# Kernel tuning notes

Measured on AMD Instinct MI355X. Metric: run time of the kernel, lower is better.

The kernel has to match this reference:

```python
import jax, jax.numpy as jnp
import numpy as np

# Dimensions
O, D, F_LSOA = 128, 128, 64      # origins, destinations, LSOA feature dim
T, FE, H = 128, 16, 64           # max seq len, edge_feature_dim, gru_hidden
NH, NO, PH = 128, 64, 128        # node_hidden, node_out, pair_hidden
P = O * D                        # number of O-D pairs


def _mlp3(x, W1, b1, W2, b2, W3, b3):
    # Linear->ReLU->Linear->ReLU->Linear (dropout is identity in eval mode)
    h = jax.nn.relu(x @ W1 + b1)
    h = jax.nn.relu(h @ W2 + b2)
    return h @ W3 + b3


def setup_inputs() -> dict:
    key = jax.random.key(0)
    ks = jax.random.split(key, 32)

    def rn(k, shape, s):
        return jax.random.normal(k, shape, dtype=jnp.float32) * s

    inp = {
        "O_feats": rn(ks[0], (O, F_LSOA), 1.0),
        "D_feats": rn(ks[1], (D, F_LSOA), 1.0),
        "seqs": rn(ks[2], (P, T, FE), 1.0),
        "lengths": jax.random.randint(ks[3], (P,), 1, T + 1, dtype=jnp.int32),
        # enc_O
        "WO1": rn(ks[4], (F_LSOA, NH), 0.05), "bO1": jnp.zeros((NH,), jnp.float32),
        "WO2": rn(ks[5], (NH, NH), 0.05),     "bO2": jnp.zeros((NH,), jnp.float32),
        "WO3": rn(ks[6], (NH, NO), 0.05),     "bO3": jnp.zeros((NO,), jnp.float32),
        # enc_D
        "WD1": rn(ks[7], (F_LSOA, NH), 0.05), "bD1": jnp.zeros((NH,), jnp.float32),
        "WD2": rn(ks[8], (NH, NH), 0.05),     "bD2": jnp.zeros((NH,), jnp.float32),
        "WD3": rn(ks[9], (NH, NO), 0.05),     "bD3": jnp.zeros((NO,), jnp.float32),
        # pair_head: 2*node_out -> pair_hidden -> 1
        "Wp1": rn(ks[10], (2 * NO, PH), 0.05), "bp1": jnp.zeros((PH,), jnp.float32),
        "Wp2": rn(ks[11], (PH, 1), 0.05),      "bp2": jnp.zeros((1,), jnp.float32),
        # GRU (gate order r, z, n as in PyTorch)
        "W_ih": rn(ks[12], (FE, 3 * H), 0.1),  "b_ih": jnp.zeros((3 * H,), jnp.float32),
        "W_hh": rn(ks[13], (H, 3 * H), 0.1),   "b_hh": jnp.zeros((3 * H,), jnp.float32),
        # seq_head
        "Ws": rn(ks[14], (H, 1), 0.1),         "bs": jnp.zeros((1,), jnp.float32),
    }
    return inp


def reference(O_feats, D_feats, seqs, lengths,
              WO1, bO1, WO2, bO2, WO3, bO3,
              WD1, bD1, WD2, bD2, WD3, bD3,
              Wp1, bp1, Wp2, bp2,
              W_ih, W_hh, b_ih, b_hh,
              Ws, bs):
    # Node encoders
    eo = _mlp3(O_feats, WO1, bO1, WO2, bO2, WO3, bO3)   # [O, NO]
    ed = _mlp3(D_feats, WD1, bD1, WD2, bD2, WD3, bD3)   # [D, NO]

    # Pairwise score: concat(eo, ed) -> MLP -> softplus
    pair_in = jnp.concatenate([
        jnp.broadcast_to(eo[:, None, :], (O, D, NO)),
        jnp.broadcast_to(ed[None, :, :], (O, D, NO)),
    ], axis=-1)                                          # [O, D, 2*NO]
    hp = jax.nn.relu(pair_in @ Wp1 + bp1)                # [O, D, PH]
    z_pair = (hp @ Wp2 + bp2)[..., 0]                    # [O, D]
    s_pair = jax.nn.softplus(z_pair)

    # Length-masked GRU over all O*D padded sequences (equiv. to pack_padded)
    xT = jnp.swapaxes(seqs, 0, 1)                        # [T, P, FE]
    h0 = jnp.zeros((P, H), jnp.float32)

    def step(h, inp):
        xt, t = inp
        gx = xt @ W_ih + b_ih                            # [P, 3H]
        gh = h @ W_hh + b_hh                             # [P, 3H]
        xr, xz, xn = jnp.split(gx, 3, axis=-1)
        hr, hz, hn = jnp.split(gh, 3, axis=-1)
        r = jax.nn.sigmoid(xr + hr)
        zg = jax.nn.sigmoid(xz + hz)
        n = jnp.tanh(xn + r * hn)
        h_new = (1.0 - zg) * n + zg * h
        h = jnp.where((t < lengths)[:, None], h_new, h)  # freeze past seq end
        return h, None

    h_last, _ = jax.lax.scan(step, h0, (xT, jnp.arange(T)))  # [P, H]

    p_seq = jax.nn.sigmoid(h_last @ Ws + bs)[:, 0].reshape(O, D)
    return jnp.sum(s_pair * p_seq)
```

## Files before the change

### kernel.cpp

```cpp
#include <hip/hip_runtime.h>
#include <hip/hip_bf16.h>

#define O_N 128
#define D_N 128
#define F_LS 64
#define T_MAX 128
#define FE_N 16
#define H_GRU 64
#define NH 128
#define NO 64
#define PH 128
#define NG 1024

typedef _Float16 f16;
typedef f16 f16x8 __attribute__((ext_vector_type(8)));
typedef f16 f16x4 __attribute__((ext_vector_type(4)));
typedef float f32x4 __attribute__((ext_vector_type(4)));

__device__ __forceinline__ float fast_sigmoid(float x) {
    return __builtin_amdgcn_rcpf(1.f + __expf(-x));
}
__device__ __forceinline__ float fast_tanh(float x) {
    return 1.f - 2.f * __builtin_amdgcn_rcpf(1.f + __expf(2.f * x));
}

__global__ __launch_bounds__(128) void k_enc(
    const float* __restrict__ O_feats, const float* __restrict__ D_feats,
    const float* __restrict__ WO1, const float* __restrict__ bO1,
    const float* __restrict__ WO2, const float* __restrict__ bO2,
    const float* __restrict__ WO3, const float* __restrict__ bO3,
    const float* __restrict__ WD1, const float* __restrict__ bD1,
    const float* __restrict__ WD2, const float* __restrict__ bD2,
    const float* __restrict__ WD3, const float* __restrict__ bD3,
    const float* __restrict__ Wp1,
    float* __restrict__ PA, float* __restrict__ PB, float* __restrict__ d_out)
{
    __shared__ float h1[NH];
    __shared__ float h2[NH];
    __shared__ float ev[NO];
    const int b = blockIdx.x;
    const int enc = b >> 7;
    const int row = b & 127;
    const int t = threadIdx.x;
    if (b == 0 && t == 0) d_out[0] = 0.f;

    const float* x  = (enc ? D_feats : O_feats) + row * F_LS;
    const float* W1 = enc ? WD1 : WO1;  const float* b1 = enc ? bD1 : bO1;
    const float* W2 = enc ? WD2 : WO2;  const float* b2 = enc ? bD2 : bO2;
    const float* W3 = enc ? WD3 : WO3;  const float* b3 = enc ? bD3 : bO3;

    float a = b1[t];
    #pragma unroll 8
    for (int k = 0; k < F_LS; ++k) a += x[k] * W1[k * NH + t];
    h1[t] = fmaxf(a, 0.f);
    __syncthreads();

    a = b2[t];
    #pragma unroll 8
    for (int k = 0; k < NH; ++k) a += h1[k] * W2[k * NH + t];
    h2[t] = fmaxf(a, 0.f);
    __syncthreads();

    if (t < NO) {
        a = b3[t];
        #pragma unroll 8
        for (int k = 0; k < NH; ++k) a += h2[k] * W3[k * NO + t];
        ev[t] = a;
    }
    __syncthreads();

    const float* Wp = Wp1 + (enc ? NO * PH : 0);
    a = 0.f;
    #pragma unroll 8
    for (int k = 0; k < NO; ++k) a += ev[k] * Wp[k * PH + t];
    (enc ? PB : PA)[row * PH + t] = a;
}

__global__ __launch_bounds__(128) void k_pair(
    const float* __restrict__ PA, const float* __restrict__ PB,
    const float* __restrict__ bp1, const float* __restrict__ Wp2,
    const float* __restrict__ bp2, float* __restrict__ s_pair)
{
    const int i = blockIdx.x;
    const int j = threadIdx.x;
    __shared__ float pa[PH];
    __shared__ float b1s[PH];
    __shared__ float w2s[PH];
    pa[j]  = PA[i * PH + j];
    b1s[j] = bp1[j];
    w2s[j] = Wp2[j];
    __syncthreads();
    const float* pb = PB + j * PH;
    float acc = 0.f;
    #pragma unroll 8
    for (int c = 0; c < PH; ++c)
        acc += w2s[c] * fmaxf(pa[c] + pb[c] + b1s[c], 0.f);
    float z = acc + bp2[0];
    float sp = fmaxf(z, 0.f) + log1pf(__expf(-fabsf(z)));
    s_pair[i * 128 + j] = sp;
}

__global__ __launch_bounds__(1024) void k_sort(
    const int* __restrict__ lengths, int* __restrict__ perm)
{
    __shared__ int cnt[130];
    __shared__ int suf[130];
    const int t = threadIdx.x;
    if (t < 130) cnt[t] = 0;
    __syncthreads();
    for (int i = t; i < 16384; i += 1024) atomicAdd(&cnt[lengths[i]], 1);
    __syncthreads();
    if (t < 130) suf[t] = cnt[t];
    __syncthreads();
    for (int d = 1; d < 130; d <<= 1) {
        int v = 0;
        if (t < 130) { v = suf[t]; if (t + d < 130) v += suf[t + d]; }
        __syncthreads();
        if (t < 130) suf[t] = v;
        __syncthreads();
    }
    if (t < 129) cnt[t] = (t + 1 < 130) ? suf[t + 1] : 0;
    __syncthreads();
    for (int i = t; i < 16384; i += 1024) {
        int pos = atomicAdd(&cnt[lengths[i]], 1);
        perm[pos] = i;
    }
}

__global__ __launch_bounds__(256, 2) void k_gru(
    const float* __restrict__ seqs, const int* __restrict__ lengths,
    const int* __restrict__ perm,
    const float* __restrict__ W_ih, const float* __restrict__ b_ih,
    const float* __restrict__ W_hh, const float* __restrict__ b_hh,
    const float* __restrict__ Ws, const float* __restrict__ bs,
    const float* __restrict__ s_pair, float* __restrict__ d_out)
{
    __shared__ __align__(16) f16 hbuf[2 * 16 * 72];
    __shared__ float red[64];
    const int tid = threadIdx.x;
    const int w  = tid >> 6;
    const int l  = tid & 63;
    const int q  = l >> 4;
    const int n  = l & 15;
    const int c  = w * 16 + n;
    const f32x4 zero4 = {0.f, 0.f, 0.f, 0.f};
    const f16x8 zero8 = {(f16)0, (f16)0, (f16)0, (f16)0, (f16)0, (f16)0, (f16)0, (f16)0};

    f16x8 wh[3][2], wi[3];
    #pragma unroll
    for (int g = 0; g < 3; ++g) {
        const int gb = g * 64;
        #pragma unroll
        for (int ks = 0; ks < 2; ++ks)
            #pragma unroll
            for (int j = 0; j < 8; ++j)
                wh[g][ks][j] = (f16)W_hh[(ks * 32 + q * 8 + j) * 192 + gb + c];
        #pragma unroll
        for (int j = 0; j < 8; ++j) {
            int k = q * 8 + j;
            wi[g][j] = (k < FE_N) ? (f16)W_ih[k * 192 + gb + c] : (f16)0.f;
        }
    }
    const float brz_r = b_ih[c] + b_hh[c];
    const float brz_z = b_ih[64 + c] + b_hh[64 + c];
    const float bxn   = b_ih[128 + c];
    const float bhn   = b_hh[128 + c];
    const float wsc   = Ws[c];
    const float bsv   = bs[0];

    for (int gi = 0; gi < 2; ++gi) {
        const int g  = gi ? (NG - 1 - (int)blockIdx.x) : (int)blockIdx.x;
        const int pb = g * 16;

        int pr[4], len[4];
        #pragma unroll
        for (int r = 0; r < 4; ++r) {
            pr[r]  = perm[pb + q * 4 + r];
            len[r] = lengths[pr[r]];
        }
        int ml = max(max(len[0], len[1]), max(len[2], len[3]));
        ml = max(ml, __shfl_xor(ml, 16));
        ml = max(ml, __shfl_xor(ml, 32));
        const int maxlen = __builtin_amdgcn_readfirstlane(ml);

        if (tid < 144) *(f16x8*)&hbuf[tid * 8] = zero8;

        const int pp = perm[pb + n];
        const float4* xp = (const float4*)(seqs + (size_t)pp * (T_MAX * FE_N)) + q * 2;
        float4 xa = {0.f, 0.f, 0.f, 0.f}, xb = xa;
        if (q < 2) { xa = xp[0]; xb = xp[1]; }

        float hold[4] = {0.f, 0.f, 0.f, 0.f};
        __syncthreads();

        for (int t = 0; t < maxlen; ++t) {
            f16x8 ax = zero8;
            if (q < 2) {
                ax[0] = (f16)xa.x; ax[1] = (f16)xa.y; ax[2] = (f16)xa.z; ax[3] = (f16)xa.w;
                ax[4] = (f16)xb.x; ax[5] = (f16)xb.y; ax[6] = (f16)xb.z; ax[7] = (f16)xb.w;
                int tn = (t + 1 < maxlen) ? (t + 1) : t;
                xa = xp[tn * 4];
                xb = xp[tn * 4 + 1];
            }
            const f16* hb  = hbuf + (t & 1) * 1152;
            f16*       hbn = hbuf + ((t + 1) & 1) * 1152;

            f16x8 ah0 = *(const f16x8*)&hb[n * 72 + q * 8];
            f16x8 ah1 = *(const f16x8*)&hb[n * 72 + 32 + q * 8];

            f32x4 axn = __builtin_amdgcn_mfma_f32_16x16x32_f16(ax, wi[2], zero4, 0, 0, 0);
            f32x4 ar  = __builtin_amdgcn_mfma_f32_16x16x32_f16(ax, wi[0], zero4, 0, 0, 0);
            ar  = __builtin_amdgcn_mfma_f32_16x16x32_f16(ah0, wh[0][0], ar, 0, 0, 0);
            ar  = __builtin_amdgcn_mfma_f32_16x16x32_f16(ah1, wh[0][1], ar, 0, 0, 0);
            f32x4 az  = __builtin_amdgcn_mfma_f32_16x16x32_f16(ax, wi[1], zero4, 0, 0, 0);
            az  = __builtin_amdgcn_mfma_f32_16x16x32_f16(ah0, wh[1][0], az, 0, 0, 0);
            az  = __builtin_amdgcn_mfma_f32_16x16x32_f16(ah1, wh[1][1], az, 0, 0, 0);
            f32x4 ahn = __builtin_amdgcn_mfma_f32_16x16x32_f16(ah0, wh[2][0], zero4, 0, 0, 0);
            ahn = __builtin_amdgcn_mfma_f32_16x16x32_f16(ah1, wh[2][1], ahn, 0, 0, 0);

            #pragma unroll
            for (int r = 0; r < 4; ++r) {
                float rg   = fast_sigmoid(ar[r] + brz_r);
                float zg   = fast_sigmoid(az[r] + brz_z);
                float nn   = fast_tanh(fmaf(rg, ahn[r] + bhn, axn[r] + bxn));
                float hnew = fmaf(zg, hold[r] - nn, nn);
                hnew = (t < len[r]) ? hnew : hold[r];
                hold[r] = hnew;
                hbn[(q * 4 + r) * 72 + c] = (f16)hnew;
            }
            __syncthreads();
        }

        float part[4];
        #pragma unroll
        for (int r = 0; r < 4; ++r) part[r] = hold[r] * wsc;
        #pragma unroll
        for (int off = 1; off < 16; off <<= 1)
            #pragma unroll
            for (int r = 0; r < 4; ++r)
                part[r] += __shfl_xor(part[r], off);
        if (n == 0) {
            #pragma unroll
            for (int r = 0; r < 4; ++r) red[w * 16 + q * 4 + r] = part[r];
        }
        __syncthreads();
        if (tid < 16) {
            float s = red[tid] + red[16 + tid] + red[32 + tid] + red[48 + tid];
            float pv = fast_sigmoid(s + bsv);
            float contrib = s_pair[perm[pb + tid]] * pv;
            #pragma unroll
            for (int off = 1; off < 16; off <<= 1)
                contrib += __shfl_xor(contrib, off);
            if (tid == 0) atomicAdd(d_out, contrib);
        }
    }
}

extern "C" void kernel_launch(void* const* d_in, const int* in_sizes, int n_in,
                              void* d_out, int out_size, void* d_ws, size_t ws_size,
                              hipStream_t stream)
{
    const float* O_feats = (const float*)d_in[0];
    const float* D_feats = (const float*)d_in[1];
    const float* seqs    = (const float*)d_in[2];
    const int*   lengths = (const int*)d_in[3];
    const float* WO1 = (const float*)d_in[4];  const float* bO1 = (const float*)d_in[5];
    const float* WO2 = (const float*)d_in[6];  const float* bO2 = (const float*)d_in[7];
    const float* WO3 = (const float*)d_in[8];  const float* bO3 = (const float*)d_in[9];
    const float* WD1 = (const float*)d_in[10]; const float* bD1 = (const float*)d_in[11];
    const float* WD2 = (const float*)d_in[12]; const float* bD2 = (const float*)d_in[13];
    const float* WD3 = (const float*)d_in[14]; const float* bD3 = (const float*)d_in[15];
    const float* Wp1 = (const float*)d_in[16]; const float* bp1 = (const float*)d_in[17];
    const float* Wp2 = (const float*)d_in[18]; const float* bp2 = (const float*)d_in[19];
    const float* W_ih = (const float*)d_in[20]; const float* b_ih = (const float*)d_in[21];
    const float* W_hh = (const float*)d_in[22]; const float* b_hh = (const float*)d_in[23];
    const float* Ws   = (const float*)d_in[24]; const float* bs   = (const float*)d_in[25];

    float* out    = (float*)d_out;
    float* PA     = (float*)d_ws;
    float* PB     = PA + 128 * 128;
    float* s_pair = PB + 128 * 128;
    int*   perm   = (int*)(s_pair + 16384);

    k_enc<<<256, 128, 0, stream>>>(O_feats, D_feats,
                                   WO1, bO1, WO2, bO2, WO3, bO3,
                                   WD1, bD1, WD2, bD2, WD3, bD3,
                                   Wp1, PA, PB, out);
    k_pair<<<128, 128, 0, stream>>>(PA, PB, bp1, Wp2, bp2, s_pair);
    k_sort<<<1, 1024, 0, stream>>>(lengths, perm);
    k_gru<<<512, 256, 0, stream>>>(seqs, lengths, perm, W_ih, b_ih, W_hh, b_hh,
                                   Ws, bs, s_pair, out);
}
```

Measured before the change: 391.6 us.

## Launch one GRU block per group with higher occupancy and pre-scaled gate weights

The GRU kernel now launches 1024 blocks, one per 16-sequence group, instead of 512 blocks that each process a paired short and long group, and raises the occupancy hint to 4 blocks per SM. Gate weights and biases are pre-scaled by -log2(e) and 2*log2(e), so the activations use raw exp2 and rcp, and the biases are folded into the MFMA accumulator initial values. This removes per-element adds and multiplies on the serial recurrence path and exposes more concurrent waves to hide latency. In exchange, it drops the load balancing from pairing groups and risks register spills under the tighter occupancy bound.

New measurement: 372.0 us. 5.0% less time.

```diff
diff --git a/kernel.cpp b/kernel.cpp
--- a/kernel.cpp
+++ b/kernel.cpp
@@ -14,14 +14,10 @@
 
 typedef _Float16 f16;
 typedef f16 f16x8 __attribute__((ext_vector_type(8)));
-typedef f16 f16x4 __attribute__((ext_vector_type(4)));
 typedef float f32x4 __attribute__((ext_vector_type(4)));
 
 __device__ __forceinline__ float fast_sigmoid(float x) {
     return __builtin_amdgcn_rcpf(1.f + __expf(-x));
-}
-__device__ __forceinline__ float fast_tanh(float x) {
-    return 1.f - 2.f * __builtin_amdgcn_rcpf(1.f + __expf(2.f * x));
 }
 
 __global__ __launch_bounds__(128) void k_enc(
@@ -127,7 +123,7 @@
     }
 }
 
-__global__ __launch_bounds__(256, 2) void k_gru(
+__global__ __launch_bounds__(256, 4) void k_gru(
     const float* __restrict__ seqs, const int* __restrict__ lengths,
     const int* __restrict__ perm,
     const float* __restrict__ W_ih, const float* __restrict__ b_ih,
@@ -135,7 +131,7 @@
     const float* __restrict__ Ws, const float* __restrict__ bs,
     const float* __restrict__ s_pair, float* __restrict__ d_out)
 {
-    __shared__ __align__(16) f16 hbuf[2 * 16 * 72];
+    __shared__ __align__(16) f16 hbuf[2 * 1152];
     __shared__ float red[64];
     const int tid = threadIdx.x;
     const int w  = tid >> 6;
@@ -143,116 +139,120 @@
     const int q  = l >> 4;
     const int n  = l & 15;
     const int c  = w * 16 + n;
-    const f32x4 zero4 = {0.f, 0.f, 0.f, 0.f};
-    const f16x8 zero8 = {(f16)0, (f16)0, (f16)0, (f16)0, (f16)0, (f16)0, (f16)0, (f16)0};
+    const int pb = blockIdx.x * 16;
+    const float S_RZ = -1.4426950408889634f;
+    const float S_N  =  2.8853900817779268f;
 
     f16x8 wh[3][2], wi[3];
     #pragma unroll
     for (int g = 0; g < 3; ++g) {
         const int gb = g * 64;
+        const float s = (g < 2) ? S_RZ : S_N;
         #pragma unroll
         for (int ks = 0; ks < 2; ++ks)
             #pragma unroll
             for (int j = 0; j < 8; ++j)
-                wh[g][ks][j] = (f16)W_hh[(ks * 32 + q * 8 + j) * 192 + gb + c];
+                wh[g][ks][j] = (f16)(W_hh[(ks * 32 + q * 8 + j) * 192 + gb + c] * s);
         #pragma unroll
         for (int j = 0; j < 8; ++j) {
             int k = q * 8 + j;
-            wi[g][j] = (k < FE_N) ? (f16)W_ih[k * 192 + gb + c] : (f16)0.f;
+            wi[g][j] = (k < FE_N) ? (f16)(W_ih[k * 192 + gb + c] * s) : (f16)0.f;
         }
     }
-    const float brz_r = b_ih[c] + b_hh[c];
-    const float brz_z = b_ih[64 + c] + b_hh[64 + c];
-    const float bxn   = b_ih[128 + c];
-    const float bhn   = b_hh[128 + c];
-    const float wsc   = Ws[c];
-    const float bsv   = bs[0];
-
-    for (int gi = 0; gi < 2; ++gi) {
-        const int g  = gi ? (NG - 1 - (int)blockIdx.x) : (int)blockIdx.x;
-        const int pb = g * 16;
-
-        int pr[4], len[4];
+    const float brz_r = S_RZ * (b_ih[c] + b_hh[c]);
+    const float brz_z = S_RZ * (b_ih[64 + c] + b_hh[64 + c]);
+    const float bhn_s = S_N * b_hh[128 + c];
+    const float bxn_s = S_N * b_ih[128 + c];
+    const f32x4 c_r  = {brz_r, brz_r, brz_r, brz_r};
+    const f32x4 c_z  = {brz_z, brz_z, brz_z, brz_z};
+    const f32x4 c_hn = {bhn_s, bhn_s, bhn_s, bhn_s};
+    const f32x4 c_xn = {bxn_s, bxn_s, bxn_s, bxn_s};
+    const float wsc  = Ws[c];
+    const float bsv  = bs[0];
+
+    int len[4];
+    #pragma unroll
+    for (int r = 0; r < 4; ++r) len[r] = lengths[perm[pb + q * 4 + r]];
+    int ml = max(max(len[0], len[1]), max(len[2], len[3]));
+    ml = max(ml, __shfl_xor(ml, 16));
+    ml = max(ml, __shfl_xor(ml, 32));
+    const int maxlen = __builtin_amdgcn_readfirstlane(ml);
+
+    {
+        f16x8 z8 = {(f16)0, (f16)0, (f16)0, (f16)0, (f16)0, (f16)0, (f16)0, (f16)0};
+        if (tid < 144) *(f16x8*)&hbuf[tid * 8] = z8;
+    }
+
+    const int pp = perm[pb + n];
+    const float4* xp = (const float4*)(seqs + (size_t)pp * (T_MAX * FE_N)) + q * 2;
+    float4 xa = {0.f, 0.f, 0.f, 0.f}, xb = xa;
+    if (q < 2) { xa = xp[0]; xb = xp[1]; }
+
+    float hold[4] = {0.f, 0.f, 0.f, 0.f};
+    const f16x8 zero8 = {(f16)0, (f16)0, (f16)0, (f16)0, (f16)0, (f16)0, (f16)0, (f16)0};
+    __syncthreads();
+
+    for (int t = 0; t < maxlen; ++t) {
+        f16x8 ax = zero8;
+        if (q < 2) {
+            ax[0] = (f16)xa.x; ax[1] = (f16)xa.y; ax[2] = (f16)xa.z; ax[3] = (f16)xa.w;
+            ax[4] = (f16)xb.x; ax[5] = (f16)xb.y; ax[6] = (f16)xb.z; ax[7] = (f16)xb.w;
+            int tn = (t + 1 < maxlen) ? (t + 1) : t;
+            xa = xp[tn * 4];
+            xb = xp[tn * 4 + 1];
+        }
+        const f16* hb  = hbuf + (t & 1) * 1152;
+        f16*       hbn = hbuf + ((t + 1) & 1) * 1152;
+
+        f16x8 ah0 = *(const f16x8*)&hb[n * 72 + q * 8];
+        f16x8 ah1 = *(const f16x8*)&hb[n * 72 + 32 + q * 8];
+
+        f32x4 ar = __builtin_amdgcn_mfma_f32_16x16x32_f16(ah0, wh[0][0], c_r, 0, 0, 0);
+        ar = __builtin_amdgcn_mfma_f32_16x16x32_f16(ah1, wh[0][1], ar, 0, 0, 0);
+        ar = __builtin_amdgcn_mfma_f32_16x16x32_f16(ax,  wi[0],    ar, 0, 0, 0);
+        f32x4 az = __builtin_amdgcn_mfma_f32_16x16x32_f16(ah0, wh[1][0], c_z, 0, 0, 0);
+        az = __builtin_amdgcn_mfma_f32_16x16x32_f16(ah1, wh[1][1], az, 0, 0, 0);
+        az = __builtin_amdgcn_mfma_f32_16x16x32_f16(ax,  wi[1],    az, 0, 0, 0);
+        f32x4 hn = __builtin_amdgcn_mfma_f32_16x16x32_f16(ah0, wh[2][0], c_hn, 0, 0, 0);
+        hn = __builtin_amdgcn_mfma_f32_16x16x32_f16(ah1, wh[2][1], hn, 0, 0, 0);
+        f32x4 xn = __builtin_amdgcn_mfma_f32_16x16x32_f16(ax, wi[2], c_xn, 0, 0, 0);
+
         #pragma unroll
         for (int r = 0; r < 4; ++r) {
-            pr[r]  = perm[pb + q * 4 + r];
-            len[r] = lengths[pr[r]];
-        }
-        int ml = max(max(len[0], len[1]), max(len[2], len[3]));
-        ml = max(ml, __shfl_xor(ml, 16));
-        ml = max(ml, __shfl_xor(ml, 32));
-        const int maxlen = __builtin_amdgcn_readfirstlane(ml);
-
-        if (tid < 144) *(f16x8*)&hbuf[tid * 8] = zero8;
-
-        const int pp = perm[pb + n];
-        const float4* xp = (const float4*)(seqs + (size_t)pp * (T_MAX * FE_N)) + q * 2;
-        float4 xa = {0.f, 0.f, 0.f, 0.f}, xb = xa;
-        if (q < 2) { xa = xp[0]; xb = xp[1]; }
-
-        float hold[4] = {0.f, 0.f, 0.f, 0.f};
-        __syncthreads();
-
-        for (int t = 0; t < maxlen; ++t) {
-            f16x8 ax = zero8;
-            if (q < 2) {
-                ax[0] = (f16)xa.x; ax[1] = (f16)xa.y; ax[2] = (f16)xa.z; ax[3] = (f16)xa.w;
-                ax[4] = (f16)xb.x; ax[5] = (f16)xb.y; ax[6] = (f16)xb.z; ax[7] = (f16)xb.w;
-                int tn = (t + 1 < maxlen) ? (t + 1) : t;
-                xa = xp[tn * 4];
-                xb = xp[tn * 4 + 1];
-            }
-            const f16* hb  = hbuf + (t & 1) * 1152;
-            f16*       hbn = hbuf + ((t + 1) & 1) * 1152;
-
-            f16x8 ah0 = *(const f16x8*)&hb[n * 72 + q * 8];
-            f16x8 ah1 = *(const f16x8*)&hb[n * 72 + 32 + q * 8];
-
-            f32x4 axn = __builtin_amdgcn_mfma_f32_16x16x32_f16(ax, wi[2], zero4, 0, 0, 0);
-            f32x4 ar  = __builtin_amdgcn_mfma_f32_16x16x32_f16(ax, wi[0], zero4, 0, 0, 0);
-            ar  = __builtin_amdgcn_mfma_f32_16x16x32_f16(ah0, wh[0][0], ar, 0, 0, 0);
-            ar  = __builtin_amdgcn_mfma_f32_16x16x32_f16(ah1, wh[0][1], ar, 0, 0, 0);
-            f32x4 az  = __builtin_amdgcn_mfma_f32_16x16x32_f16(ax, wi[1], zero4, 0, 0, 0);
-            az  = __builtin_amdgcn_mfma_f32_16x16x32_f16(ah0, wh[1][0], az, 0, 0, 0);
-            az  = __builtin_amdgcn_mfma_f32_16x16x32_f16(ah1, wh[1][1], az, 0, 0, 0);
-            f32x4 ahn = __builtin_amdgcn_mfma_f32_16x16x32_f16(ah0, wh[2][0], zero4, 0, 0, 0);
-            ahn = __builtin_amdgcn_mfma_f32_16x16x32_f16(ah1, wh[2][1], ahn, 0, 0, 0);
-
-            #pragma unroll
-            for (int r = 0; r < 4; ++r) {
-                float rg   = fast_sigmoid(ar[r] + brz_r);
-                float zg   = fast_sigmoid(az[r] + brz_z);
-                float nn   = fast_tanh(fmaf(rg, ahn[r] + bhn, axn[r] + bxn));
-                float hnew = fmaf(zg, hold[r] - nn, nn);
-                hnew = (t < len[r]) ? hnew : hold[r];
-                hold[r] = hnew;
-                hbn[(q * 4 + r) * 72 + c] = (f16)hnew;
-            }
-            __syncthreads();
-        }
-
-        float part[4];
-        #pragma unroll
-        for (int r = 0; r < 4; ++r) part[r] = hold[r] * wsc;
-        #pragma unroll
-        for (int off = 1; off < 16; off <<= 1)
-            #pragma unroll
-            for (int r = 0; r < 4; ++r)
-                part[r] += __shfl_xor(part[r], off);
-        if (n == 0) {
-            #pragma unroll
-            for (int r = 0; r < 4; ++r) red[w * 16 + q * 4 + r] = part[r];
+            float rg    = __builtin_amdgcn_rcpf(1.f + __builtin_amdgcn_exp2f(ar[r]));
+            float zg    = __builtin_amdgcn_rcpf(1.f + __builtin_amdgcn_exp2f(az[r]));
+            float inner = fmaf(rg, hn[r], xn[r]);
+            float nn    = fmaf(-2.f, __builtin_amdgcn_rcpf(1.f + __builtin_amdgcn_exp2f(inner)), 1.f);
+            float hv    = hold[r];
+            float hnew  = fmaf(zg, hv - nn, nn);
+            hnew = (t < len[r]) ? hnew : hv;
+            hold[r] = hnew;
+            hbn[(q * 4 + r) * 72 + c] = (f16)hnew;
         }
         __syncthreads();
-        if (tid < 16) {
-            float s = red[tid] + red[16 + tid] + red[32 + tid] + red[48 + tid];
-            float pv = fast_sigmoid(s + bsv);
-            float contrib = s_pair[perm[pb + tid]] * pv;
-            #pragma unroll
-            for (int off = 1; off < 16; off <<= 1)
-                contrib += __shfl_xor(contrib, off);
-            if (tid == 0) atomicAdd(d_out, contrib);
-        }
+    }
+
+    float part[4];
+    #pragma unroll
+    for (int r = 0; r < 4; ++r) part[r] = hold[r] * wsc;
+    #pragma unroll
+    for (int off = 1; off < 16; off <<= 1)
+        #pragma unroll
+        for (int r = 0; r < 4; ++r)
+            part[r] += __shfl_xor(part[r], off);
+    if (n == 0) {
+        #pragma unroll
+        for (int r = 0; r < 4; ++r) red[w * 16 + q * 4 + r] = part[r];
+    }
+    __syncthreads();
+    if (tid < 16) {
+        float s = red[tid] + red[16 + tid] + red[32 + tid] + red[48 + tid];
+        float pv = fast_sigmoid(s + bsv);
+        float contrib = s_pair[perm[pb + tid]] * pv;
+        #pragma unroll
+        for (int off = 1; off < 16; off <<= 1)
+            contrib += __shfl_xor(contrib, off);
+        if (tid == 0) atomicAdd(d_out, contrib);
     }
 }
 
@@ -288,6 +288,6 @@
                                    Wp1, PA, PB, out);
     k_pair<<<128, 128, 0, stream>>>(PA, PB, bp1, Wp2, bp2, s_pair);
     k_sort<<<1, 1024, 0, stream>>>(lengths, perm);
-    k_gru<<<512, 256, 0, stream>>>(seqs, lengths, perm, W_ih, b_ih, W_hh, b_hh,
-                                   Ws, bs, s_pair, out);
-}
+    k_gru<<<1024, 256, 0, stream>>>(seqs, lengths, perm, W_ih, b_ih, W_hh, b_hh,
+                                    Ws, bs, s_pair, out);
+}
```
